# Optimization experiments

Hardware: AMD Instinct MI355X
Metric: run time of the kernel (lower is better)

The kernel has to match this reference:

```python
import jax, jax.numpy as jnp
import numpy as np

N_NODES = 50000
N_EDGES = 800000
IN_FEATS = 128
HID = 64
HEADS = 3
NUM_CLASSES = 8
ATTN_SLOPE = 0.2   # DGL GATConv leaky_relu slope on attention logits
ACT_SLOPE = 0.01   # nn.LeakyReLU default


def setup_inputs() -> dict:
    key = jax.random.key(0)
    ks = jax.random.split(key, 40)
    inp = {}
    inp["x"] = jax.random.normal(ks[0], (N_NODES, IN_FEATS), dtype=jnp.float32)
    inp["src"] = jax.random.randint(ks[1], (N_EDGES,), 0, N_NODES)
    inp["dst"] = jax.random.randint(ks[2], (N_EDGES,), 0, N_NODES)
    dims_in = [IN_FEATS, HID, HID, HID, HID]
    i = 3
    for l, din in enumerate(dims_in, start=1):
        inp[f"W{l}"] = jax.random.normal(ks[i], (din, HEADS * HID), dtype=jnp.float32) / np.float32(np.sqrt(din)); i += 1
        inp[f"b{l}"] = jnp.zeros((HEADS * HID,), dtype=jnp.float32)
        inp[f"al{l}"] = jax.random.normal(ks[i], (HEADS, HID), dtype=jnp.float32) * 0.1; i += 1
        inp[f"ar{l}"] = jax.random.normal(ks[i], (HEADS, HID), dtype=jnp.float32) * 0.1; i += 1
    inp["Wo"] = jax.random.normal(ks[i], (HID, NUM_CLASSES), dtype=jnp.float32) / np.float32(np.sqrt(HID)); i += 1
    inp["bo"] = jnp.zeros((NUM_CLASSES,), dtype=jnp.float32)
    return inp


def _gatconv(h, W, b, al, ar, src, dst):
    # h: [N, din] -> feat: [N, H, F]
    feat = (h @ W).reshape(N_NODES, HEADS, HID)
    el = jnp.einsum('nhf,hf->nh', feat, al)   # [N, H]
    er = jnp.einsum('nhf,hf->nh', feat, ar)   # [N, H]
    e = jax.nn.leaky_relu(el[src] + er[dst], ATTN_SLOPE)        # [E, H]
    # numerically-stable edge softmax segmented by destination node
    m = jax.ops.segment_max(e, dst, num_segments=N_NODES)      # [N, H]
    ex = jnp.exp(e - m[dst])                                   # [E, H]
    denom = jax.ops.segment_sum(ex, dst, num_segments=N_NODES)  # [N, H]
    alpha = ex / denom[dst]                                    # [E, H]
    msg = alpha[:, :, None] * feat[src]                        # [E, H, F]
    out = jax.ops.segment_sum(msg, dst, num_segments=N_NODES)  # [N, H, F]
    return out + b.reshape(HEADS, HID)


def reference(x, src, dst,
              W1, b1, al1, ar1,
              W2, b2, al2, ar2,
              W3, b3, al3, ar3,
              W4, b4, al4, ar4,
              W5, b5, al5, ar5,
              Wo, bo):
    layers = [(W1, b1, al1, ar1), (W2, b2, al2, ar2), (W3, b3, al3, ar3),
              (W4, b4, al4, ar4), (W5, b5, al5, ar5)]
    h = x
    for (W, b, al, ar) in layers:
        h = jax.nn.leaky_relu(_gatconv(h, W, b, al, ar, src, dst), ACT_SLOPE)
        h = h.mean(axis=1)  # mean over heads -> [N, F]
    return h @ Wo + bo      # [N, num_classes]
```

## Files before the change

### kernel.cpp

```cpp
#include <hip/hip_runtime.h>
#include <hip/hip_fp16.h>
#include <cstdint>

#define N_NODES 50000
#define N_EDGES 800000
#define IN_FEATS 128
#define HID 64
#define HEADS 3
#define NUM_CLASSES 8
#define ATTN_SLOPE 0.2f
#define ACT_SLOPE 0.01f

typedef _Float16 half8 __attribute__((ext_vector_type(8)));
typedef float f32x4 __attribute__((ext_vector_type(4)));

__device__ __forceinline__ float lrelu(float x, float s) { return x > 0.f ? x : s * x; }

__global__ void k_deg(const int* __restrict__ dst, int* __restrict__ deg, int E) {
    int i = blockIdx.x * blockDim.x + threadIdx.x;
    if (i < E) atomicAdd(&deg[dst[i]], 1);
}

__global__ __launch_bounds__(256) void k_scan1(const int* __restrict__ deg, int* __restrict__ off,
                                               int* __restrict__ bsum, int n) {
    __shared__ int wtot[4];
    int tid = threadIdx.x;
    int lane = tid & 63, wid = tid >> 6;
    int base = blockIdx.x * 2048 + tid * 8;
    int v[8];
    if (base + 8 <= n) {
        int4 a = *(const int4*)&deg[base];
        int4 b = *(const int4*)&deg[base + 4];
        v[0] = a.x; v[1] = a.y; v[2] = a.z; v[3] = a.w;
        v[4] = b.x; v[5] = b.y; v[6] = b.z; v[7] = b.w;
    } else {
#pragma unroll
        for (int j = 0; j < 8; ++j) v[j] = (base + j < n) ? deg[base + j] : 0;
    }
    int s[8];
    s[0] = v[0];
#pragma unroll
    for (int j = 1; j < 8; ++j) s[j] = s[j - 1] + v[j];
    int t = s[7];
    int incl = t;
    for (int o = 1; o < 64; o <<= 1) {
        int u = __shfl_up(incl, o);
        if (lane >= o) incl += u;
    }
    int excl = incl - t;
    if (lane == 63) wtot[wid] = incl;
    __syncthreads();
    int wprefix = 0;
    for (int w = 0; w < wid; ++w) wprefix += wtot[w];
    int base_off = wprefix + excl;
#pragma unroll
    for (int j = 0; j < 8; ++j)
        if (base + j < n) off[base + j] = base_off + s[j] - v[j];
    if (tid == 0) bsum[blockIdx.x] = wtot[0] + wtot[1] + wtot[2] + wtot[3];
}

__global__ __launch_bounds__(64) void k_scan2(int* __restrict__ bsum, int nb) {
    int tid = threadIdx.x;
    int v = (tid < nb) ? bsum[tid] : 0;
    int incl = v;
    for (int o = 1; o < 64; o <<= 1) {
        int u = __shfl_up(incl, o);
        if (tid >= o) incl += u;
    }
    if (tid < nb) bsum[tid] = incl - v;
}

__global__ __launch_bounds__(256) void k_scan3(int* __restrict__ off, const int* __restrict__ bsum,
                                               int n, int E) {
    int i = blockIdx.x * blockDim.x + threadIdx.x;
    if (i < n) off[i] += bsum[i >> 11];
    if (i == 0) off[n] = E;
}

__global__ void k_fill(const int* __restrict__ src, const int* __restrict__ dst,
                       const int* __restrict__ off, int* __restrict__ cur,
                       int* __restrict__ ssrc, int E) {
    int i = blockIdx.x * blockDim.x + threadIdx.x;
    if (i < E) {
        int d = dst[i];
        int p = atomicAdd(&cur[d], 1);
        ssrc[off[d] + p] = src[i];
    }
}

__global__ __launch_bounds__(256) void k_xcast(const float* __restrict__ x, _Float16* __restrict__ xh, int n8) {
    int i = blockIdx.x * blockDim.x + threadIdx.x;
    if (i < n8) {
        float4 a = *(const float4*)&x[i * 8];
        float4 b = *(const float4*)&x[i * 8 + 4];
        _Float16 v[8] = {(_Float16)a.x, (_Float16)a.y, (_Float16)a.z, (_Float16)a.w,
                         (_Float16)b.x, (_Float16)b.y, (_Float16)b.z, (_Float16)b.w};
        *(uint4*)&xh[i * 8] = *(uint4*)v;
    }
}

__global__ __launch_bounds__(256) void k_wcast(const float* __restrict__ W1, const float* __restrict__ W2,
                                               const float* __restrict__ W3, const float* __restrict__ W4,
                                               const float* __restrict__ W5, _Float16* __restrict__ Wt) {
    int i = blockIdx.x * blockDim.x + threadIdx.x;
    if (i >= 24576 + 4 * 12288) return;
    const float* W; int din; int idx; _Float16* out;
    if (i < 24576) { W = W1; din = 128; idx = i; out = Wt; }
    else {
        int j = i - 24576; int l = j / 12288; idx = j % 12288;
        W = (l == 0) ? W2 : (l == 1) ? W3 : (l == 2) ? W4 : W5;
        din = 64;
        out = Wt + 24576 + l * 12288;
    }
    int col = idx / din, k = idx % din;
    out[idx] = (_Float16)W[k * 192 + col];
}

__global__ __launch_bounds__(256) void k_gemm(const _Float16* __restrict__ h, const _Float16* __restrict__ Wt,
                                              const float* __restrict__ al, const float* __restrict__ ar,
                                              _Float16* __restrict__ feat,
                                              float* __restrict__ el, float* __restrict__ er,
                                              int N, int din) {
    __shared__ __align__(16) _Float16 Hl[128 * 136];
    __shared__ __align__(16) _Float16 Wl[64 * 136];
    const int K = din;
    const int LD = K + 8;
    const int KC = K >> 3;
    int tid = threadIdx.x;
    int row0 = blockIdx.x * 128;
    int head = blockIdx.y;
    int c0 = head * 64;

    for (int i = tid; i < 64 * KC; i += 256) {
        int col = i / KC, c8 = i % KC;
        *(uint4*)&Wl[col * LD + c8 * 8] = *(const uint4*)&Wt[(size_t)(c0 + col) * K + c8 * 8];
    }
    for (int i = tid; i < 128 * KC; i += 256) {
        int r = i / KC, c8 = i % KC;
        int row = row0 + r;
        uint4 v = make_uint4(0, 0, 0, 0);
        if (row < N) v = *(const uint4*)&h[(size_t)row * K + c8 * 8];
        *(uint4*)&Hl[r * LD + c8 * 8] = v;
    }
    __syncthreads();

    int wid = tid >> 6, lane = tid & 63;
    int l15 = lane & 15;
    int koff = (lane >> 4) * 8;
    int wr0 = wid * 32;

    f32x4 acc[2][4] = {};
    int nkb = K >> 5;
    for (int kb = 0; kb < nkb; ++kb) {
        int kbase = kb * 32 + koff;
        half8 a0 = *(half8*)&Hl[(wr0 + l15) * LD + kbase];
        half8 a1 = *(half8*)&Hl[(wr0 + 16 + l15) * LD + kbase];
        half8 b0 = *(half8*)&Wl[(l15) * LD + kbase];
        half8 b1 = *(half8*)&Wl[(16 + l15) * LD + kbase];
        half8 b2 = *(half8*)&Wl[(32 + l15) * LD + kbase];
        half8 b3 = *(half8*)&Wl[(48 + l15) * LD + kbase];
        acc[0][0] = __builtin_amdgcn_mfma_f32_16x16x32_f16(a0, b0, acc[0][0], 0, 0, 0);
        acc[0][1] = __builtin_amdgcn_mfma_f32_16x16x32_f16(a0, b1, acc[0][1], 0, 0, 0);
        acc[0][2] = __builtin_amdgcn_mfma_f32_16x16x32_f16(a0, b2, acc[0][2], 0, 0, 0);
        acc[0][3] = __builtin_amdgcn_mfma_f32_16x16x32_f16(a0, b3, acc[0][3], 0, 0, 0);
        acc[1][0] = __builtin_amdgcn_mfma_f32_16x16x32_f16(a1, b0, acc[1][0], 0, 0, 0);
        acc[1][1] = __builtin_amdgcn_mfma_f32_16x16x32_f16(a1, b1, acc[1][1], 0, 0, 0);
        acc[1][2] = __builtin_amdgcn_mfma_f32_16x16x32_f16(a1, b2, acc[1][2], 0, 0, 0);
        acc[1][3] = __builtin_amdgcn_mfma_f32_16x16x32_f16(a1, b3, acc[1][3], 0, 0, 0);
    }

    float alv[4], arv[4];
#pragma unroll
    for (int ct = 0; ct < 4; ++ct) {
        alv[ct] = al[c0 + ct * 16 + l15];
        arv[ct] = ar[c0 + ct * 16 + l15];
    }

#pragma unroll
    for (int rt = 0; rt < 2; ++rt) {
#pragma unroll
        for (int r = 0; r < 4; ++r) {
            int row = row0 + wr0 + rt * 16 + (lane >> 4) * 4 + r;
            bool ok = (row < N);
            float c0v = acc[rt][0][r], c1v = acc[rt][1][r], c2v = acc[rt][2][r], c3v = acc[rt][3][r];
            if (ok) {
                size_t base = (size_t)row * 192 + c0;
                feat[base + l15]      = (_Float16)c0v;
                feat[base + 16 + l15] = (_Float16)c1v;
                feat[base + 32 + l15] = (_Float16)c2v;
                feat[base + 48 + l15] = (_Float16)c3v;
            }
            float pl = c0v * alv[0] + c1v * alv[1] + c2v * alv[2] + c3v * alv[3];
            float pr = c0v * arv[0] + c1v * arv[1] + c2v * arv[2] + c3v * arv[3];
            for (int o = 1; o < 16; o <<= 1) {
                pl += __shfl_xor(pl, o);
                pr += __shfl_xor(pr, o);
            }
            if (ok && l15 == 0) {
                el[row * HEADS + head] = pl;
                er[row * HEADS + head] = pr;
            }
        }
    }
}

__global__ __launch_bounds__(64) void k_agg(const int* __restrict__ off, const int* __restrict__ ssrc,
                                            const float* __restrict__ el, const float* __restrict__ er,
                                            const __half* __restrict__ feat, const float* __restrict__ b,
                                            __half* __restrict__ hout, int N) {
    __shared__ float4 ebuf[64];
    int wid = blockIdx.x;
    int lane = threadIdx.x;
    if (wid >= N) return;
    int start = off[wid], end = off[wid + 1];
    int cnt = end - start;
    float er0 = er[wid * HEADS + 0];
    float er1 = er[wid * HEADS + 1];
    float er2 = er[wid * HEADS + 2];
    float acc0 = 0.f, acc1 = 0.f, acc2 = 0.f;
    float den0 = 0.f, den1 = 0.f, den2 = 0.f;

    if (cnt <= 64) {
        int s0 = 0;
        float ea = -3.4e38f, eb = -3.4e38f, ec = -3.4e38f;
        if (lane < cnt) {
            s0 = ssrc[start + lane];
            ea = lrelu(el[s0 * HEADS + 0] + er0, ATTN_SLOPE);
            eb = lrelu(el[s0 * HEADS + 1] + er1, ATTN_SLOPE);
            ec = lrelu(el[s0 * HEADS + 2] + er2, ATTN_SLOPE);
        }
        float ma = ea, mb = eb, mc = ec;
        for (int o = 32; o > 0; o >>= 1) {
            ma = fmaxf(ma, __shfl_xor(ma, o));
            mb = fmaxf(mb, __shfl_xor(mb, o));
            mc = fmaxf(mc, __shfl_xor(mc, o));
        }
        float xa = (lane < cnt) ? __expf(ea - ma) : 0.f;
        float xb = (lane < cnt) ? __expf(eb - mb) : 0.f;
        float xc = (lane < cnt) ? __expf(ec - mc) : 0.f;
        float da = xa, db = xb, dc = xc;
        for (int o = 32; o > 0; o >>= 1) {
            da += __shfl_xor(da, o);
            db += __shfl_xor(db, o);
            dc += __shfl_xor(dc, o);
        }
        den0 = da; den1 = db; den2 = dc;
        ebuf[lane] = make_float4(__int_as_float(s0), xa, xb, xc);
        int t = 0;
        for (; t + 4 <= cnt; t += 4) {
            float4 v0 = ebuf[t + 0];
            float4 v1 = ebuf[t + 1];
            float4 v2 = ebuf[t + 2];
            float4 v3 = ebuf[t + 3];
            const __half* f0 = feat + (size_t)__float_as_int(v0.x) * 192 + lane;
            const __half* f1 = feat + (size_t)__float_as_int(v1.x) * 192 + lane;
            const __half* f2 = feat + (size_t)__float_as_int(v2.x) * 192 + lane;
            const __half* f3 = feat + (size_t)__float_as_int(v3.x) * 192 + lane;
            float p00 = __half2float(f0[0]), p01 = __half2float(f0[64]), p02 = __half2float(f0[128]);
            float p10 = __half2float(f1[0]), p11 = __half2float(f1[64]), p12 = __half2float(f1[128]);
            float p20 = __half2float(f2[0]), p21 = __half2float(f2[64]), p22 = __half2float(f2[128]);
            float p30 = __half2float(f3[0]), p31 = __half2float(f3[64]), p32 = __half2float(f3[128]);
            acc0 += v0.y * p00; acc1 += v0.z * p01; acc2 += v0.w * p02;
            acc0 += v1.y * p10; acc1 += v1.z * p11; acc2 += v1.w * p12;
            acc0 += v2.y * p20; acc1 += v2.z * p21; acc2 += v2.w * p22;
            acc0 += v3.y * p30; acc1 += v3.z * p31; acc2 += v3.w * p32;
        }
        for (; t < cnt; ++t) {
            float4 v = ebuf[t];
            const __half* fr = feat + (size_t)__float_as_int(v.x) * 192 + lane;
            acc0 += v.y * __half2float(fr[0]);
            acc1 += v.z * __half2float(fr[64]);
            acc2 += v.w * __half2float(fr[128]);
        }
    } else {
        float ma = -3.4e38f, mb = -3.4e38f, mc = -3.4e38f;
        for (int j = start + lane; j < end; j += 64) {
            int s = ssrc[j];
            ma = fmaxf(ma, lrelu(el[s * HEADS + 0] + er0, ATTN_SLOPE));
            mb = fmaxf(mb, lrelu(el[s * HEADS + 1] + er1, ATTN_SLOPE));
            mc = fmaxf(mc, lrelu(el[s * HEADS + 2] + er2, ATTN_SLOPE));
        }
        for (int o = 32; o > 0; o >>= 1) {
            ma = fmaxf(ma, __shfl_xor(ma, o));
            mb = fmaxf(mb, __shfl_xor(mb, o));
            mc = fmaxf(mc, __shfl_xor(mc, o));
        }
        float da = 0.f, db = 0.f, dc = 0.f;
        for (int j0 = start; j0 < end; j0 += 64) {
            int jj = j0 + lane;
            int s0 = 0;
            float xa = 0.f, xb = 0.f, xc = 0.f;
            if (jj < end) {
                s0 = ssrc[jj];
                xa = __expf(lrelu(el[s0 * HEADS + 0] + er0, ATTN_SLOPE) - ma);
                xb = __expf(lrelu(el[s0 * HEADS + 1] + er1, ATTN_SLOPE) - mb);
                xc = __expf(lrelu(el[s0 * HEADS + 2] + er2, ATTN_SLOPE) - mc);
            }
            da += xa; db += xb; dc += xc;
            ebuf[lane] = make_float4(__int_as_float(s0), xa, xb, xc);
            int c = min(64, end - j0);
            int t = 0;
            for (; t + 4 <= c; t += 4) {
                float4 v0 = ebuf[t + 0];
                float4 v1 = ebuf[t + 1];
                float4 v2 = ebuf[t + 2];
                float4 v3 = ebuf[t + 3];
                const __half* f0 = feat + (size_t)__float_as_int(v0.x) * 192 + lane;
                const __half* f1 = feat + (size_t)__float_as_int(v1.x) * 192 + lane;
                const __half* f2 = feat + (size_t)__float_as_int(v2.x) * 192 + lane;
                const __half* f3 = feat + (size_t)__float_as_int(v3.x) * 192 + lane;
                float p00 = __half2float(f0[0]), p01 = __half2float(f0[64]), p02 = __half2float(f0[128]);
                float p10 = __half2float(f1[0]), p11 = __half2float(f1[64]), p12 = __half2float(f1[128]);
                float p20 = __half2float(f2[0]), p21 = __half2float(f2[64]), p22 = __half2float(f2[128]);
                float p30 = __half2float(f3[0]), p31 = __half2float(f3[64]), p32 = __half2float(f3[128]);
                acc0 += v0.y * p00; acc1 += v0.z * p01; acc2 += v0.w * p02;
                acc0 += v1.y * p10; acc1 += v1.z * p11; acc2 += v1.w * p12;
                acc0 += v2.y * p20; acc1 += v2.z * p21; acc2 += v2.w * p22;
                acc0 += v3.y * p30; acc1 += v3.z * p31; acc2 += v3.w * p32;
            }
            for (; t < c; ++t) {
                float4 v = ebuf[t];
                const __half* fr = feat + (size_t)__float_as_int(v.x) * 192 + lane;
                acc0 += v.y * __half2float(fr[0]);
                acc1 += v.z * __half2float(fr[64]);
                acc2 += v.w * __half2float(fr[128]);
            }
        }
        for (int o = 32; o > 0; o >>= 1) {
            da += __shfl_xor(da, o);
            db += __shfl_xor(db, o);
            dc += __shfl_xor(dc, o);
        }
        den0 = da; den1 = db; den2 = dc;
    }

    float v0 = (cnt > 0) ? acc0 / den0 : 0.f;
    float v1 = (cnt > 0) ? acc1 / den1 : 0.f;
    float v2 = (cnt > 0) ? acc2 / den2 : 0.f;
    float hsum = lrelu(v0 + b[lane], ACT_SLOPE)
               + lrelu(v1 + b[64 + lane], ACT_SLOPE)
               + lrelu(v2 + b[128 + lane], ACT_SLOPE);
    hout[wid * 64 + lane] = __float2half(hsum * (1.f / 3.f));
}

__global__ __launch_bounds__(256) void k_out(const __half* __restrict__ h, const float* __restrict__ Wo,
                                             const float* __restrict__ bo, float* __restrict__ out, int N) {
    __shared__ float Hl[32][65];
    __shared__ float Wl[64 * 8];
    int tid = threadIdx.x;
    int n0 = blockIdx.x * 32;
    for (int i = tid; i < 32 * 64; i += 256) {
        int r = i >> 6, k = i & 63;
        Hl[r][k] = (n0 + r < N) ? __half2float(h[(n0 + r) * 64 + k]) : 0.f;
    }
    for (int i = tid; i < 512; i += 256) Wl[i] = Wo[i];
    __syncthreads();
    int r = tid >> 3, c = tid & 7;
    float acc = 0.f;
    for (int k = 0; k < 64; ++k) acc += Hl[r][k] * Wl[k * 8 + c];
    int row = n0 + r;
    if (row < N) out[row * 8 + c] = acc + bo[c];
}

extern "C" void kernel_launch(void* const* d_in, const int* in_sizes, int n_in,
                              void* d_out, int out_size, void* d_ws, size_t ws_size,
                              hipStream_t stream) {
    const float* x  = (const float*)d_in[0];
    const int* src  = (const int*)d_in[1];
    const int* dst  = (const int*)d_in[2];
    const float *W[5], *b[5], *al[5], *ar[5];
    for (int l = 0; l < 5; ++l) {
        W[l]  = (const float*)d_in[3 + l * 4];
        b[l]  = (const float*)d_in[4 + l * 4];
        al[l] = (const float*)d_in[5 + l * 4];
        ar[l] = (const float*)d_in[6 + l * 4];
    }
    const float* Wo = (const float*)d_in[23];
    const float* bo = (const float*)d_in[24];
    float* out = (float*)d_out;

    char* ws = (char*)d_ws;
    auto alloc = [&](size_t bytes) {
        char* p = ws;
        ws += (bytes + 255) & ~size_t(255);
        return p;
    };
    _Float16* feat = (_Float16*)alloc(sizeof(_Float16) * (size_t)N_NODES * 192);
    float* el      = (float*)alloc(sizeof(float) * (size_t)N_NODES * HEADS);
    float* er      = (float*)alloc(sizeof(float) * (size_t)N_NODES * HEADS);
    _Float16* xh   = (_Float16*)alloc(sizeof(_Float16) * (size_t)N_NODES * IN_FEATS);
    _Float16* h0   = (_Float16*)alloc(sizeof(_Float16) * (size_t)N_NODES * 64);
    _Float16* h1   = (_Float16*)alloc(sizeof(_Float16) * (size_t)N_NODES * 64);
    _Float16* wt   = (_Float16*)alloc(sizeof(_Float16) * (24576 + 4 * 12288));
    int* deg    = (int*)alloc(sizeof(int) * N_NODES);
    int* off    = (int*)alloc(sizeof(int) * (N_NODES + 1));
    int* cur    = (int*)alloc(sizeof(int) * N_NODES);
    int* ssrc   = (int*)alloc(sizeof(int) * N_EDGES);
    int* bsum   = (int*)alloc(sizeof(int) * 64);

    const int NB = (N_NODES + 2047) / 2048;
    (void)hipMemsetAsync(deg, 0, sizeof(int) * N_NODES, stream);
    (void)hipMemsetAsync(cur, 0, sizeof(int) * N_NODES, stream);
    k_deg<<<(N_EDGES + 255) / 256, 256, 0, stream>>>(dst, deg, N_EDGES);
    k_scan1<<<NB, 256, 0, stream>>>(deg, off, bsum, N_NODES);
    k_scan2<<<1, 64, 0, stream>>>(bsum, NB);
    k_scan3<<<(N_NODES + 255) / 256, 256, 0, stream>>>(off, bsum, N_NODES, N_EDGES);
    k_fill<<<(N_EDGES + 255) / 256, 256, 0, stream>>>(src, dst, off, cur, ssrc, N_EDGES);
    k_xcast<<<(N_NODES * IN_FEATS / 8 + 255) / 256, 256, 0, stream>>>(x, xh, N_NODES * IN_FEATS / 8);
    k_wcast<<<(24576 + 4 * 12288 + 255) / 256, 256, 0, stream>>>(W[0], W[1], W[2], W[3], W[4], wt);

    const _Float16* hin = xh;
    _Float16* hbuf[2] = {h0, h1};
    const _Float16* wts[5] = {wt, wt + 24576, wt + 24576 + 12288, wt + 24576 + 2 * 12288, wt + 24576 + 3 * 12288};
    int din = IN_FEATS;
    for (int l = 0; l < 5; ++l) {
        dim3 ggrid((N_NODES + 127) / 128, HEADS);
        k_gemm<<<ggrid, 256, 0, stream>>>(hin, wts[l], al[l], ar[l], feat, el, er, N_NODES, din);
        _Float16* hn = hbuf[l & 1];
        k_agg<<<N_NODES, 64, 0, stream>>>(off, ssrc, el, er,
                                          (const __half*)feat, b[l],
                                          (__half*)hn, N_NODES);
        hin = hn;
        din = HID;
    }
    k_out<<<(N_NODES + 31) / 32, 256, 0, stream>>>((const __half*)hin, Wo, bo, out, N_NODES);
}
```

Measured before the change: 519.2 us.

## Compute all heads per GEMM block to reuse loaded input tile

The GEMM kernel now covers all three heads in one 384-thread block: each wave pair handles one head and half the 128 rows, each wave holding a 4x4 grid of MFMA accumulators. This replaces the per-head grid dimension, so each input row tile is loaded from global memory once instead of three times. K is processed in 64-wide chunks with a synchronisation between chunks. In exchange each wave holds more accumulator registers, and there are fewer blocks with only one 64-wide K chunk in flight at a time.

```diff
diff --git a/kernel.cpp b/kernel.cpp
--- a/kernel.cpp
+++ b/kernel.cpp
@@ -116,57 +116,56 @@
     out[idx] = (_Float16)W[k * 192 + col];
 }
 
-__global__ __launch_bounds__(256) void k_gemm(const _Float16* __restrict__ h, const _Float16* __restrict__ Wt,
+__global__ __launch_bounds__(384) void k_gemm(const _Float16* __restrict__ h, const _Float16* __restrict__ Wt,
                                               const float* __restrict__ al, const float* __restrict__ ar,
                                               _Float16* __restrict__ feat,
                                               float* __restrict__ el, float* __restrict__ er,
                                               int N, int din) {
-    __shared__ __align__(16) _Float16 Hl[128 * 136];
-    __shared__ __align__(16) _Float16 Wl[64 * 136];
-    const int K = din;
-    const int LD = K + 8;
-    const int KC = K >> 3;
+    __shared__ __align__(16) _Float16 Hl[128 * 72];
+    __shared__ __align__(16) _Float16 Wl[192 * 72];
+    const int LD = 72;
     int tid = threadIdx.x;
     int row0 = blockIdx.x * 128;
-    int head = blockIdx.y;
+    int wid = tid >> 6, lane = tid & 63;
+    int head = wid >> 1, rh = wid & 1;
     int c0 = head * 64;
-
-    for (int i = tid; i < 64 * KC; i += 256) {
-        int col = i / KC, c8 = i % KC;
-        *(uint4*)&Wl[col * LD + c8 * 8] = *(const uint4*)&Wt[(size_t)(c0 + col) * K + c8 * 8];
-    }
-    for (int i = tid; i < 128 * KC; i += 256) {
-        int r = i / KC, c8 = i % KC;
-        int row = row0 + r;
-        uint4 v = make_uint4(0, 0, 0, 0);
-        if (row < N) v = *(const uint4*)&h[(size_t)row * K + c8 * 8];
-        *(uint4*)&Hl[r * LD + c8 * 8] = v;
-    }
-    __syncthreads();
-
-    int wid = tid >> 6, lane = tid & 63;
     int l15 = lane & 15;
     int koff = (lane >> 4) * 8;
-    int wr0 = wid * 32;
-
-    f32x4 acc[2][4] = {};
-    int nkb = K >> 5;
-    for (int kb = 0; kb < nkb; ++kb) {
-        int kbase = kb * 32 + koff;
-        half8 a0 = *(half8*)&Hl[(wr0 + l15) * LD + kbase];
-        half8 a1 = *(half8*)&Hl[(wr0 + 16 + l15) * LD + kbase];
-        half8 b0 = *(half8*)&Wl[(l15) * LD + kbase];
-        half8 b1 = *(half8*)&Wl[(16 + l15) * LD + kbase];
-        half8 b2 = *(half8*)&Wl[(32 + l15) * LD + kbase];
-        half8 b3 = *(half8*)&Wl[(48 + l15) * LD + kbase];
-        acc[0][0] = __builtin_amdgcn_mfma_f32_16x16x32_f16(a0, b0, acc[0][0], 0, 0, 0);
-        acc[0][1] = __builtin_amdgcn_mfma_f32_16x16x32_f16(a0, b1, acc[0][1], 0, 0, 0);
-        acc[0][2] = __builtin_amdgcn_mfma_f32_16x16x32_f16(a0, b2, acc[0][2], 0, 0, 0);
-        acc[0][3] = __builtin_amdgcn_mfma_f32_16x16x32_f16(a0, b3, acc[0][3], 0, 0, 0);
-        acc[1][0] = __builtin_amdgcn_mfma_f32_16x16x32_f16(a1, b0, acc[1][0], 0, 0, 0);
-        acc[1][1] = __builtin_amdgcn_mfma_f32_16x16x32_f16(a1, b1, acc[1][1], 0, 0, 0);
-        acc[1][2] = __builtin_amdgcn_mfma_f32_16x16x32_f16(a1, b2, acc[1][2], 0, 0, 0);
-        acc[1][3] = __builtin_amdgcn_mfma_f32_16x16x32_f16(a1, b3, acc[1][3], 0, 0, 0);
+    int wr0 = rh * 64;
+
+    f32x4 acc[4][4] = {};
+
+    for (int k0 = 0; k0 < din; k0 += 64) {
+        if (k0 > 0) __syncthreads();
+        for (int i = tid; i < 192 * 8; i += 384) {
+            int col = i >> 3, c8 = i & 7;
+            *(uint4*)&Wl[col * LD + c8 * 8] = *(const uint4*)&Wt[(size_t)col * din + k0 + c8 * 8];
+        }
+        for (int i = tid; i < 128 * 8; i += 384) {
+            int r = i >> 3, c8 = i & 7;
+            int row = row0 + r;
+            uint4 v = make_uint4(0, 0, 0, 0);
+            if (row < N) v = *(const uint4*)&h[(size_t)row * din + k0 + c8 * 8];
+            *(uint4*)&Hl[r * LD + c8 * 8] = v;
+        }
+        __syncthreads();
+
+#pragma unroll
+        for (int kb = 0; kb < 2; ++kb) {
+            int kbase = kb * 32 + koff;
+            half8 b0 = *(half8*)&Wl[(c0 + l15) * LD + kbase];
+            half8 b1 = *(half8*)&Wl[(c0 + 16 + l15) * LD + kbase];
+            half8 b2 = *(half8*)&Wl[(c0 + 32 + l15) * LD + kbase];
+            half8 b3 = *(half8*)&Wl[(c0 + 48 + l15) * LD + kbase];
+#pragma unroll
+            for (int rt = 0; rt < 4; ++rt) {
+                half8 a = *(half8*)&Hl[(wr0 + rt * 16 + l15) * LD + kbase];
+                acc[rt][0] = __builtin_amdgcn_mfma_f32_16x16x32_f16(a, b0, acc[rt][0], 0, 0, 0);
+                acc[rt][1] = __builtin_amdgcn_mfma_f32_16x16x32_f16(a, b1, acc[rt][1], 0, 0, 0);
+                acc[rt][2] = __builtin_amdgcn_mfma_f32_16x16x32_f16(a, b2, acc[rt][2], 0, 0, 0);
+                acc[rt][3] = __builtin_amdgcn_mfma_f32_16x16x32_f16(a, b3, acc[rt][3], 0, 0, 0);
+            }
+        }
     }
 
     float alv[4], arv[4];
@@ -177,7 +176,7 @@
     }
 
 #pragma unroll
-    for (int rt = 0; rt < 2; ++rt) {
+    for (int rt = 0; rt < 4; ++rt) {
 #pragma unroll
         for (int r = 0; r < 4; ++r) {
             int row = row0 + wr0 + rt * 16 + (lane >> 4) * 4 + r;
@@ -414,8 +413,7 @@
     const _Float16* wts[5] = {wt, wt + 24576, wt + 24576 + 12288, wt + 24576 + 2 * 12288, wt + 24576 + 3 * 12288};
     int din = IN_FEATS;
     for (int l = 0; l < 5; ++l) {
-        dim3 ggrid((N_NODES + 127) / 128, HEADS);
-        k_gemm<<<ggrid, 256, 0, stream>>>(hin, wts[l], al[l], ar[l], feat, el, er, N_NODES, din);
+        k_gemm<<<(N_NODES + 127) / 128, 384, 0, stream>>>(hin, wts[l], al[l], ar[l], feat, el, er, N_NODES, din);
         _Float16* hn = hbuf[l & 1];
         k_agg<<<N_NODES, 64, 0, stream>>>(off, ssrc, el, er,
                                           (const __half*)feat, b[l],
```

Measured after the change: 521.7 us. Within noise of the previous version (+0.5%).
